# Kernel tuning notes

Measured on AMD Instinct MI355X. Metric: run time of the kernel, lower is better.

The kernel has to match this reference:

```python
import jax, jax.numpy as jnp
import numpy as np

NEG_SLOPE = 0.2  # PyG GATConv default negative_slope


def gat_layer(x, W, a_src, a_dst, bias, src, dst, num_nodes):
    # x: [N, Fin], W: [Fin, H*C], a_src/a_dst: [H, C], bias: [C]
    H, C = a_src.shape
    h = (x @ W).reshape(num_nodes, H, C)                      # [N, H, C]
    alpha_src = jnp.einsum('nhc,hc->nh', h, a_src)            # [N, H]
    alpha_dst = jnp.einsum('nhc,hc->nh', h, a_dst)            # [N, H]
    e = jax.nn.leaky_relu(alpha_src[src] + alpha_dst[dst], NEG_SLOPE)  # [E, H]
    # segment softmax over incoming edges of each destination node
    m = jax.ops.segment_max(e, dst, num_segments=num_nodes)  # [N, H]
    p = jnp.exp(e - m[dst])
    denom = jax.ops.segment_sum(p, dst, num_segments=num_nodes)
    alpha = p / denom[dst]                                    # [E, H]
    out = jax.ops.segment_sum(h[src] * alpha[:, :, None], dst,
                              num_segments=num_nodes)         # [N, H, C]
    return out.mean(axis=1) + bias                            # concat=False -> mean


def setup_inputs() -> dict:
    key = jax.random.key(0)
    ks = jax.random.split(key, 8)
    N, E, F, H = 20000, 640000, 128, 4
    s = 0.1  # weight init scale
    return {
        'x': jax.random.normal(ks[0], (N, F), jnp.float32),
        'W1': jax.random.normal(ks[1], (F, H * F), jnp.float32) * s,
        'a_src1': jax.random.normal(ks[2], (H, F), jnp.float32) * s,
        'a_dst1': jax.random.normal(ks[3], (H, F), jnp.float32) * s,
        'b1': jnp.zeros((F,), jnp.float32),
        'W2': jax.random.normal(ks[4], (F, F), jnp.float32) * s,
        'a_src2': jax.random.normal(ks[5], (1, F), jnp.float32) * s,
        'a_dst2': jax.random.normal(ks[6], (1, F), jnp.float32) * s,
        'b2': jnp.zeros((F,), jnp.float32),
        'edge_index': jax.random.randint(ks[7], (2, E), 0, N, jnp.int32),
    }


def reference(x, W1, a_src1, a_dst1, b1, W2, a_src2, a_dst2, b2, edge_index):
    N = x.shape[0]
    loop = jnp.arange(N, dtype=edge_index.dtype)  # add_self_loops=True (PyG default)
    src = jnp.concatenate([edge_index[0], loop])
    dst = jnp.concatenate([edge_index[1], loop])
    h = jax.nn.elu(gat_layer(x, W1, a_src1, a_dst1, b1, src, dst, N))
    out = jax.nn.elu(gat_layer(h, W2, a_src2, a_dst2, b2, src, dst, N))
    return out
```

## Files before the change

### kernel.cpp

```cpp
#include <hip/hip_runtime.h>
#include <hip/hip_bf16.h>


typedef short v8s __attribute__((ext_vector_type(8)));
typedef float v4f __attribute__((ext_vector_type(4)));
typedef float v2f __attribute__((ext_vector_type(2)));

template <int K> struct IC { static constexpr int value = K; };

constexpr int MAXD = 128;

__device__ __forceinline__ void bf2x(unsigned int u, float& lo, float& hi) {
    union { unsigned int i; float f; } a, b;
    a.i = u << 16;
    b.i = u & 0xffff0000u;
    lo = a.f;
    hi = b.f;
}
__device__ __forceinline__ v2f bf2p(unsigned int u) {
    union { unsigned int i; float f; } a, b;
    a.i = u << 16;
    b.i = u & 0xffff0000u;
    return (v2f){a.f, b.f};
}
__device__ __forceinline__ unsigned short f2bf(float f) {
    union { float f; unsigned int i; } v;
    v.f = f;
    unsigned int lsb = (v.i >> 16) & 1u;
    v.i += 0x7fffu + lsb;
    return (unsigned short)(v.i >> 16);
}
__device__ __forceinline__ unsigned int pack2(float a, float b) {
    return (unsigned int)f2bf(a) | ((unsigned int)f2bf(b) << 16);
}

__global__ void fused_prep_kernel(const float* __restrict__ x,
                                  const float* __restrict__ W1, const float* __restrict__ W2,
                                  const float* __restrict__ as1v, const float* __restrict__ ad1v,
                                  const float* __restrict__ as2v, const float* __restrict__ ad2v,
                                  unsigned short* __restrict__ xb,
                                  unsigned short* __restrict__ Bt1,
                                  unsigned short* __restrict__ Bt2,
                                  float* __restrict__ wsrc1, float* __restrict__ wdst1,
                                  float* __restrict__ wsrc2, float* __restrict__ wdst2,
                                  int* __restrict__ cnt, int* __restrict__ slot,
                                  float* __restrict__ as2, float* __restrict__ ad2, int N) {
    const int Bcast = (N * 32 + 255) / 256;
    int b = blockIdx.x;
    if (b < Bcast) {
        int i = (b * 256 + threadIdx.x) * 4;
        if (i + 3 < N * 128) {
            float4 v = *(const float4*)&x[i];
            ushort4 o;
            o.x = f2bf(v.x);
            o.y = f2bf(v.y);
            o.z = f2bf(v.z);
            o.w = f2bf(v.w);
            *(ushort4*)&xb[i] = o;
        } else {
            for (; i < N * 128; ++i) xb[i] = f2bf(x[i]);
        }
        return;
    }
    b -= Bcast;
    if (b < 256) {
        int i = b * 256 + threadIdx.x;
        int c = i >> 9;
        int r = i & 511;
        int h = r >> 7, k = r & 127;
        Bt1[i] = f2bf(W1[(size_t)k * 512 + (h << 7) + c] * 0.25f);
        return;
    }
    b -= 256;
    if (b < 64) {
        int i = b * 256 + threadIdx.x;
        int c = i >> 7, k = i & 127;
        Bt2[i] = f2bf(W2[(size_t)k * 128 + c]);
        return;
    }
    b -= 64;
    if (b < 2) {
        int i = b * 256 + threadIdx.x;
        int h = i >> 7, k = i & 127;
        const float* wr = W1 + (size_t)k * 512 + (h << 7);
        const float* as_ = as1v + (h << 7);
        const float* ad_ = ad1v + (h << 7);
        float s1 = 0.f, s2 = 0.f;
        for (int c = 0; c < 128; ++c) {
            float wv = wr[c];
            s1 += wv * as_[c];
            s2 += wv * ad_[c];
        }
        wsrc1[i] = s1;
        wdst1[i] = s2;
        return;
    }
    b -= 2;
    if (b < 1) {
        int k = threadIdx.x;
        if (k < 128) {
            const float* wr = W2 + (size_t)k * 128;
            float s1 = 0.f, s2 = 0.f;
            for (int c = 0; c < 128; ++c) {
                float wv = wr[c];
                s1 += wv * as2v[c];
                s2 += wv * ad2v[c];
            }
            wsrc2[k] = s1;
            wdst2[k] = s2;
        }
        return;
    }
    b -= 1;
    {
        int i = b * 256 + threadIdx.x;
        if (i < N) {
            cnt[i] = 1;
            slot[(size_t)i * MAXD] = i;
            as2[i] = 0.f;
            ad2[i] = 0.f;
        }
    }
}

__launch_bounds__(256)
__global__ void fill_alpha_kernel(const int* __restrict__ src, const int* __restrict__ dst,
                                  int* __restrict__ cnt, int* __restrict__ slot, int E,
                                  const unsigned int* __restrict__ xrow,
                                  const float* __restrict__ wsrc, const float* __restrict__ wdst,
                                  float* __restrict__ asrc, float* __restrict__ adst, int N,
                                  int Bfill) {
    if ((int)blockIdx.x < Bfill) {
        int i = (blockIdx.x * 256 + threadIdx.x) * 4;
        if (i + 3 < E) {
            int4 s4 = *(const int4*)&src[i];
            int4 d4 = *(const int4*)&dst[i];
            int p0 = atomicAdd(&cnt[d4.x], 1);
            int p1 = atomicAdd(&cnt[d4.y], 1);
            int p2 = atomicAdd(&cnt[d4.z], 1);
            int p3 = atomicAdd(&cnt[d4.w], 1);
            if (p0 < MAXD) slot[(size_t)d4.x * MAXD + p0] = s4.x;
            if (p1 < MAXD) slot[(size_t)d4.y * MAXD + p1] = s4.y;
            if (p2 < MAXD) slot[(size_t)d4.z * MAXD + p2] = s4.z;
            if (p3 < MAXD) slot[(size_t)d4.w * MAXD + p3] = s4.w;
        } else {
            for (; i < E; ++i) {
                int d = dst[i];
                int pos = atomicAdd(&cnt[d], 1);
                if (pos < MAXD) slot[(size_t)d * MAXD + pos] = src[i];
            }
        }
        return;
    }
    constexpr int H = 4;
    __shared__ float s_wv[2 * H * 128];
    for (int i = threadIdx.x; i < 2 * H * 128; i += 256)
        s_wv[i] = (i < H * 128) ? wsrc[i] : wdst[i - H * 128];
    __syncthreads();
    const int wid = threadIdx.x >> 6, lane = threadIdx.x & 63;
    const int n = (blockIdx.x - Bfill) * 4 + wid;
    if (n >= N) return;
    unsigned int u = xrow[(size_t)n * 64 + lane];
    float f0, f1;
    bf2x(u, f0, f1);
    float s1[H], s2[H];
#pragma unroll
    for (int h = 0; h < H; ++h) {
        float2 ws = *(const float2*)&s_wv[h * 128 + 2 * lane];
        float2 wd = *(const float2*)&s_wv[H * 128 + h * 128 + 2 * lane];
        s1[h] = f0 * ws.x + f1 * ws.y;
        s2[h] = f0 * wd.x + f1 * wd.y;
    }
#pragma unroll
    for (int off = 32; off; off >>= 1)
#pragma unroll
        for (int h = 0; h < H; ++h) {
            s1[h] += __shfl_xor(s1[h], off);
            s2[h] += __shfl_xor(s2[h], off);
        }
    if (lane == 0) {
#pragma unroll
        for (int h = 0; h < H; ++h) {
            asrc[(size_t)n * H + h] = s1[h];
            adst[(size_t)n * H + h] = s2[h];
        }
    }
}

template <int H, int NPB>
__launch_bounds__(64 * NPB, 4)
__global__ void gat_gather_kernel(const uint4* __restrict__ xrow4,
                                  const float* __restrict__ asrc,
                                  const float* __restrict__ adst,
                                  const int* __restrict__ cnt,
                                  const int* __restrict__ slot,
                                  uint4* __restrict__ Sb4,
                                  int N) {
    static_assert(H == 4 || H == 1, "H");
    const int wid = threadIdx.x >> 6, lane = threadIdx.x & 63;
    const int q = lane >> 4, l16 = lane & 15;
    const int n = blockIdx.x * NPB + wid;
    if (n >= N) return;

    __shared__ int s_src_all[NPB][64];
    __shared__ float s_w_all[NPB][64 * H];
    int* s_src = s_src_all[wid];
    float* s_w = s_w_all[wid];

    const int base = n * MAXD;
    const int deg = min(cnt[n], MAXD);

    float adst_n[H];
#pragma unroll
    for (int h = 0; h < H; ++h) adst_n[h] = adst[(size_t)n * H + h];

    float sum_h[H] = {};
    v2f acc[4 * H];
#pragma unroll
    for (int i = 0; i < 4 * H; ++i) acc[i] = (v2f){0.f, 0.f};

    auto do_batch = [&](int j0, auto kc) {
        constexpr int KK = decltype(kc)::value;
        int ss[KK];
        uint4 d[KK];
#pragma unroll
        for (int k = 0; k < KK; ++k) ss[k] = s_src[j0 + k * 4 + q];
#pragma unroll
        for (int k = 0; k < KK; ++k) d[k] = xrow4[(size_t)ss[k] * 16 + l16];
#pragma unroll
        for (int k = 0; k < KK; ++k) {
            v2f f2[4];
            f2[0] = bf2p(d[k].x);
            f2[1] = bf2p(d[k].y);
            f2[2] = bf2p(d[k].z);
            f2[3] = bf2p(d[k].w);
            if constexpr (H == 4) {
                float4 w = *(const float4*)&s_w[(j0 + k * 4 + q) * 4];
                v2f w0 = (v2f){w.x, w.x}, w1 = (v2f){w.y, w.y};
                v2f w2 = (v2f){w.z, w.z}, w3 = (v2f){w.w, w.w};
#pragma unroll
                for (int j = 0; j < 4; ++j) {
                    acc[j] += w0 * f2[j];
                    acc[4 + j] += w1 * f2[j];
                    acc[8 + j] += w2 * f2[j];
                    acc[12 + j] += w3 * f2[j];
                }
            } else {
                float w = s_w[j0 + k * 4 + q];
                v2f w0 = (v2f){w, w};
#pragma unroll
                for (int j = 0; j < 4; ++j) acc[j] += w0 * f2[j];
            }
        }
    };

    for (int i0 = 0; i0 < deg; i0 += 64) {
        const int cntc = min(64, deg - i0);
        {
            const bool valid = lane < cntc;
            int idx = i0 + (valid ? lane : (cntc - 1));
            int s = slot[base + idx];
            s_src[lane] = s;
            if constexpr (H == 4) {
                float4 av = ((const float4*)asrc)[s];
                float ev[4] = {av.x, av.y, av.z, av.w};
#pragma unroll
                for (int hh = 0; hh < 4; ++hh) {
                    float e = ev[hh] + adst_n[hh];
                    e = e > 0.f ? e : 0.2f * e;
                    float wv = valid ? __expf(e) : 0.f;
                    s_w[lane * 4 + hh] = wv;
                    sum_h[hh] += wv;
                }
            } else {
                float e = asrc[s] + adst_n[0];
                e = e > 0.f ? e : 0.2f * e;
                float wv = valid ? __expf(e) : 0.f;
                s_w[lane] = wv;
                sum_h[0] += wv;
            }
        }
        __threadfence_block();

        int j0 = 0;
        for (; j0 + 32 <= cntc; j0 += 32) do_batch(j0, IC<8>{});
        const int rem = cntc - j0;
        if (rem > 0) {
            switch ((rem + 3) >> 2) {
                case 1: do_batch(j0, IC<1>{}); break;
                case 2: do_batch(j0, IC<2>{}); break;
                case 3: do_batch(j0, IC<3>{}); break;
                case 4: do_batch(j0, IC<4>{}); break;
                case 5: do_batch(j0, IC<5>{}); break;
                case 6: do_batch(j0, IC<6>{}); break;
                case 7: do_batch(j0, IC<7>{}); break;
                default: do_batch(j0, IC<8>{}); break;
            }
        }
    }

#pragma unroll
    for (int i = 0; i < 4 * H; ++i) {
        acc[i][0] += __shfl_xor(acc[i][0], 16);
        acc[i][1] += __shfl_xor(acc[i][1], 16);
        acc[i][0] += __shfl_xor(acc[i][0], 32);
        acc[i][1] += __shfl_xor(acc[i][1], 32);
    }
#pragma unroll
    for (int off = 32; off; off >>= 1)
#pragma unroll
        for (int h = 0; h < H; ++h) sum_h[h] += __shfl_xor(sum_h[h], off);

    if constexpr (H == 4) {
#pragma unroll
        for (int h = 0; h < 4; ++h) {
            if (q == h) {
                float rd = 1.0f / sum_h[h];
                uint4 o;
                o.x = pack2(acc[h * 4 + 0][0] * rd, acc[h * 4 + 0][1] * rd);
                o.y = pack2(acc[h * 4 + 1][0] * rd, acc[h * 4 + 1][1] * rd);
                o.z = pack2(acc[h * 4 + 2][0] * rd, acc[h * 4 + 2][1] * rd);
                o.w = pack2(acc[h * 4 + 3][0] * rd, acc[h * 4 + 3][1] * rd);
                Sb4[(size_t)n * 64 + h * 16 + l16] = o;
            }
        }
    } else {
        if (q == 0) {
            float rd = 1.0f / sum_h[0];
            uint4 o;
            o.x = pack2(acc[0][0] * rd, acc[0][1] * rd);
            o.y = pack2(acc[1][0] * rd, acc[1][1] * rd);
            o.z = pack2(acc[2][0] * rd, acc[2][1] * rd);
            o.w = pack2(acc[3][0] * rd, acc[3][1] * rd);
            Sb4[(size_t)n * 16 + l16] = o;
        }
    }
}

__device__ __forceinline__ void store_out(float* p, float v) { *p = v; }
__device__ __forceinline__ void store_out(unsigned short* p, float v) { *p = f2bf(v); }

template <typename OT, bool ELU, bool FUSE_A2>
__launch_bounds__(256)
__global__ void gemm_bias_act_kernel(const unsigned short* __restrict__ A,
                                     const unsigned short* __restrict__ Bt,
                                     const float* __restrict__ bias,
                                     OT* __restrict__ C,
                                     const float* __restrict__ ws2,
                                     const float* __restrict__ wd2,
                                     float* __restrict__ as2, float* __restrict__ ad2,
                                     int M, int Nout, int K) {
    constexpr int BK = 32;
    __shared__ unsigned short As[64][40];
    __shared__ unsigned short Bs[64][40];

    const int tid = threadIdx.x;
    const int w = tid >> 6;
    const int lane = tid & 63;
    const int m16 = lane & 15;
    const int kg = lane >> 4;
    const int m0 = blockIdx.y * 64;
    const int n0 = blockIdx.x * 64;

    v4f acc[4];
#pragma unroll
    for (int i = 0; i < 4; ++i) acc[i] = (v4f){0.f, 0.f, 0.f, 0.f};

    const int srow = tid >> 2;
    const int sseg = tid & 3;
    const int arow_g = min(m0 + srow, M - 1);
    const unsigned short* Ap = &A[(size_t)arow_g * K + sseg * 8];
    const unsigned short* Bp = &Bt[(size_t)(n0 + srow) * K + sseg * 8];

    for (int k0 = 0; k0 < K; k0 += BK) {
        uint4 av = *(const uint4*)(Ap + k0);
        uint4 bv = *(const uint4*)(Bp + k0);
        __syncthreads();
        *(uint4*)&As[srow][sseg * 8] = av;
        *(uint4*)&Bs[srow][sseg * 8] = bv;
        __syncthreads();
        v8s a = *(const v8s*)&As[w * 16 + m16][kg * 8];
#pragma unroll
        for (int i = 0; i < 4; ++i) {
            v8s b = *(const v8s*)&Bs[i * 16 + m16][kg * 8];
            acc[i] = __builtin_amdgcn_mfma_f32_16x16x32_bf16(a, b, acc[i], 0, 0, 0);
        }
    }

    float pr_s[4] = {}, pr_d[4] = {};
#pragma unroll
    for (int i = 0; i < 4; ++i) {
        const int col = n0 + i * 16 + m16;
        const float bv = bias[col];
        float w2s = 0.f, w2d = 0.f;
        if constexpr (FUSE_A2) {
            w2s = ws2[col];
            w2d = wd2[col];
        }
#pragma unroll
        for (int r = 0; r < 4; ++r) {
            int row = m0 + w * 16 + kg * 4 + r;
            if (row < M) {
                float val = acc[i][r] + bv;
                if constexpr (ELU) val = val > 0.f ? val : (__expf(val) - 1.0f);
                store_out(&C[(size_t)row * Nout + col], val);
                if constexpr (FUSE_A2) {
                    pr_s[r] += val * w2s;
                    pr_d[r] += val * w2d;
                }
            }
        }
    }
    if constexpr (FUSE_A2) {
#pragma unroll
        for (int off = 1; off < 16; off <<= 1)
#pragma unroll
            for (int r = 0; r < 4; ++r) {
                pr_s[r] += __shfl_xor(pr_s[r], off);
                pr_d[r] += __shfl_xor(pr_d[r], off);
            }
        if (m16 == 0) {
#pragma unroll
            for (int r = 0; r < 4; ++r) {
                int row = m0 + w * 16 + kg * 4 + r;
                if (row < M) {
                    atomicAdd(&as2[row], pr_s[r]);
                    atomicAdd(&ad2[row], pr_d[r]);
                }
            }
        }
    }
}


extern "C" void kernel_launch(void* const* d_in, const int* in_sizes, int n_in,
                              void* d_out, int out_size, void* d_ws, size_t ws_size,
                              hipStream_t stream) {
    const float* x = (const float*)d_in[0];
    const float* W1 = (const float*)d_in[1];
    const float* a_src1 = (const float*)d_in[2];
    const float* a_dst1 = (const float*)d_in[3];
    const float* b1 = (const float*)d_in[4];
    const float* W2 = (const float*)d_in[5];
    const float* a_src2 = (const float*)d_in[6];
    const float* a_dst2 = (const float*)d_in[7];
    const float* b2 = (const float*)d_in[8];
    const int* edge = (const int*)d_in[9];
    float* out = (float*)d_out;

    constexpr int F = 128, H = 4;
    const int N = in_sizes[0] / F;
    const int E = in_sizes[9] / 2;

    char* ws = (char*)d_ws;
    size_t o = 0;
    auto take = [&](size_t bytes) {
        char* p = ws + o;
        o = (o + bytes + 255) & ~(size_t)255;
        return p;
    };
    int* cnt = (int*)take((size_t)N * 4);
    int* slot = (int*)take((size_t)N * MAXD * 4);
    unsigned short* xb = (unsigned short*)take((size_t)N * F * 2);
    unsigned short* Bt1 = (unsigned short*)take((size_t)F * H * F * 2);
    unsigned short* Bt2 = (unsigned short*)take((size_t)F * F * 2);
    float* wsrc1 = (float*)take((size_t)H * F * 4);
    float* wdst1 = (float*)take((size_t)H * F * 4);
    float* wsrc2 = (float*)take((size_t)F * 4);
    float* wdst2 = (float*)take((size_t)F * 4);
    float* as1 = (float*)take((size_t)N * H * 4);
    float* ad1 = (float*)take((size_t)N * H * 4);
    unsigned short* Sb1 = (unsigned short*)take((size_t)N * H * F * 2);
    unsigned short* h2b = (unsigned short*)take((size_t)N * F * 2);
    float* as2 = (float*)take((size_t)N * 4);
    float* ad2 = (float*)take((size_t)N * 4);
    unsigned short* S2b = (unsigned short*)take((size_t)N * F * 2);
    (void)ws_size;

    const int* esrc = edge;
    const int* edst = edge + E;

    const int Bcast = (N * 32 + 255) / 256;
    const int Bzero = (N + 255) / 256;
    hipLaunchKernelGGL(fused_prep_kernel, dim3(Bcast + 256 + 64 + 2 + 1 + Bzero), dim3(256), 0,
                       stream, x, W1, W2, a_src1, a_dst1, a_src2, a_dst2, xb, Bt1, Bt2, wsrc1,
                       wdst1, wsrc2, wdst2, cnt, slot, as2, ad2, N);

    const int Bfill = (E / 4 + 255) / 256;
    const int Balpha = (N + 3) / 4;
    hipLaunchKernelGGL(fill_alpha_kernel, dim3(Bfill + Balpha), dim3(256), 0, stream, esrc, edst,
                       cnt, slot, E, (const unsigned int*)xb, wsrc1, wdst1, as1, ad1, N, Bfill);

    hipLaunchKernelGGL((gat_gather_kernel<H, 4>), dim3((N + 3) / 4), dim3(256), 0, stream,
                       (const uint4*)xb, as1, ad1, cnt, slot, (uint4*)Sb1, N);
    hipLaunchKernelGGL((gemm_bias_act_kernel<unsigned short, true, true>),
                       dim3(F / 64, (N + 63) / 64), dim3(256), 0, stream, Sb1, Bt1, b1, h2b,
                       wsrc2, wdst2, as2, ad2, N, F, H * F);

    hipLaunchKernelGGL((gat_gather_kernel<1, 4>), dim3((N + 3) / 4), dim3(256), 0, stream,
                       (const uint4*)h2b, as2, ad2, cnt, slot, (uint4*)S2b, N);
    hipLaunchKernelGGL((gemm_bias_act_kernel<float, true, false>), dim3(F / 64, (N + 63) / 64),
                       dim3(256), 0, stream, S2b, Bt2, b2, out, nullptr, nullptr, nullptr,
                       nullptr, N, F, F);
}
```

Baseline: 206.7 us.

## Build adjacency via two-pass binned counting sort with 16-bit slot indices

Replaces the global-atomic scatter that filled per-destination slot lists with a binned partition: a histogram over 64-node bins, a per-block partition into a bin buffer through shared-memory staging, and a per-bin build step that fills slot lists in LDS and writes them out coalesced. Slot indices shrink to 16-bit, halving slot traffic in both gather kernels. This removes random global atomics and scattered 4-byte writes, but adds two kernel launches and an extra pass over the edges. Packing limits source ids to 15 bits and bins to 11 bits, which holds only for N up to 32768.

```diff
diff --git a/kernel.cpp b/kernel.cpp
--- a/kernel.cpp
+++ b/kernel.cpp
@@ -9,6 +9,8 @@
 template <int K> struct IC { static constexpr int value = K; };
 
 constexpr int MAXD = 128;
+constexpr int EPB = 4096;
+constexpr int BINW = 64;
 
 __device__ __forceinline__ void bf2x(unsigned int u, float& lo, float& hi) {
     union { unsigned int i; float f; } a, b;
@@ -32,6 +34,18 @@
 }
 __device__ __forceinline__ unsigned int pack2(float a, float b) {
     return (unsigned int)f2bf(a) | ((unsigned int)f2bf(b) << 16);
+}
+
+__device__ __forceinline__ void scan512_incl(unsigned int* a, int tid) {
+#pragma unroll
+    for (int off = 1; off < 512; off <<= 1) {
+        unsigned int v0 = (tid >= off) ? a[tid - off] : 0u;
+        unsigned int v1 = a[tid + 256 - off];
+        __syncthreads();
+        a[tid] += v0;
+        a[tid + 256] += v1;
+        __syncthreads();
+    }
 }
 
 __global__ void fused_prep_kernel(const float* __restrict__ x,
@@ -43,8 +57,10 @@
                                   unsigned short* __restrict__ Bt2,
                                   float* __restrict__ wsrc1, float* __restrict__ wdst1,
                                   float* __restrict__ wsrc2, float* __restrict__ wdst2,
-                                  int* __restrict__ cnt, int* __restrict__ slot,
-                                  float* __restrict__ as2, float* __restrict__ ad2, int N) {
+                                  unsigned int* __restrict__ ghist,
+                                  unsigned int* __restrict__ bincur,
+                                  float* __restrict__ as2, float* __restrict__ ad2,
+                                  int N, int NB) {
     const int Bcast = (N * 32 + 255) / 256;
     int b = blockIdx.x;
     if (b < Bcast) {
@@ -115,41 +131,45 @@
     {
         int i = b * 256 + threadIdx.x;
         if (i < N) {
-            cnt[i] = 1;
-            slot[(size_t)i * MAXD] = i;
             as2[i] = 0.f;
             ad2[i] = 0.f;
         }
+        if (i < NB) {
+            ghist[i] = 0u;
+            bincur[i] = 0u;
+        }
     }
 }
 
 __launch_bounds__(256)
-__global__ void fill_alpha_kernel(const int* __restrict__ src, const int* __restrict__ dst,
-                                  int* __restrict__ cnt, int* __restrict__ slot, int E,
+__global__ void hist_alpha_kernel(const int* __restrict__ dst, int E,
+                                  unsigned int* __restrict__ ghist, int NB, int Bh,
                                   const unsigned int* __restrict__ xrow,
                                   const float* __restrict__ wsrc, const float* __restrict__ wdst,
-                                  float* __restrict__ asrc, float* __restrict__ adst, int N,
-                                  int Bfill) {
-    if ((int)blockIdx.x < Bfill) {
-        int i = (blockIdx.x * 256 + threadIdx.x) * 4;
-        if (i + 3 < E) {
-            int4 s4 = *(const int4*)&src[i];
-            int4 d4 = *(const int4*)&dst[i];
-            int p0 = atomicAdd(&cnt[d4.x], 1);
-            int p1 = atomicAdd(&cnt[d4.y], 1);
-            int p2 = atomicAdd(&cnt[d4.z], 1);
-            int p3 = atomicAdd(&cnt[d4.w], 1);
-            if (p0 < MAXD) slot[(size_t)d4.x * MAXD + p0] = s4.x;
-            if (p1 < MAXD) slot[(size_t)d4.y * MAXD + p1] = s4.y;
-            if (p2 < MAXD) slot[(size_t)d4.z * MAXD + p2] = s4.z;
-            if (p3 < MAXD) slot[(size_t)d4.w * MAXD + p3] = s4.w;
-        } else {
-            for (; i < E; ++i) {
-                int d = dst[i];
-                int pos = atomicAdd(&cnt[d], 1);
-                if (pos < MAXD) slot[(size_t)d * MAXD + pos] = src[i];
-            }
-        }
+                                  float* __restrict__ asrc, float* __restrict__ adst, int N) {
+    if ((int)blockIdx.x < Bh) {
+        __shared__ unsigned int bh[512];
+        const int tid = threadIdx.x;
+        bh[tid] = 0u;
+        bh[tid + 256] = 0u;
+        __syncthreads();
+        const int e0 = blockIdx.x * EPB;
+        const int ne = min(EPB, E - e0);
+#pragma unroll
+        for (int k = 0; k < 4; ++k) {
+            int rel = (k * 256 + tid) * 4;
+            if (rel < ne) {
+                int4 d4 = *(const int4*)&dst[e0 + rel];
+                atomicAdd(&bh[(unsigned int)d4.x >> 6], 1u);
+                atomicAdd(&bh[(unsigned int)d4.y >> 6], 1u);
+                atomicAdd(&bh[(unsigned int)d4.z >> 6], 1u);
+                atomicAdd(&bh[(unsigned int)d4.w >> 6], 1u);
+            }
+        }
+        __syncthreads();
+        unsigned int c0 = bh[tid], c1 = bh[tid + 256];
+        if (tid < NB && c0) atomicAdd(&ghist[tid], c0);
+        if (tid + 256 < NB && c1) atomicAdd(&ghist[tid + 256], c1);
         return;
     }
     constexpr int H = 4;
@@ -158,7 +178,7 @@
         s_wv[i] = (i < H * 128) ? wsrc[i] : wdst[i - H * 128];
     __syncthreads();
     const int wid = threadIdx.x >> 6, lane = threadIdx.x & 63;
-    const int n = (blockIdx.x - Bfill) * 4 + wid;
+    const int n = (blockIdx.x - Bh) * 4 + wid;
     if (n >= N) return;
     unsigned int u = xrow[(size_t)n * 64 + lane];
     float f0, f1;
@@ -185,6 +205,109 @@
             adst[(size_t)n * H + h] = s2[h];
         }
     }
+}
+
+__launch_bounds__(256)
+__global__ void csr_partition_kernel(const int* __restrict__ src, const int* __restrict__ dst,
+                                     const unsigned int* __restrict__ ghist,
+                                     unsigned int* __restrict__ bincur,
+                                     unsigned int* __restrict__ binBuf, int E, int NB) {
+    __shared__ unsigned int bh[512];
+    __shared__ unsigned int g[512];
+    __shared__ unsigned int sres[512];
+    __shared__ unsigned int stg[EPB];
+    const int tid = threadIdx.x;
+    const int e0 = blockIdx.x * EPB;
+    const int ne = min(EPB, E - e0);
+    bh[tid] = 0u;
+    bh[tid + 256] = 0u;
+    g[tid] = (tid < NB) ? ghist[tid] : 0u;
+    g[tid + 256] = (tid + 256 < NB) ? ghist[tid + 256] : 0u;
+    __syncthreads();
+
+    unsigned int pk[16], ps[16];
+#pragma unroll
+    for (int k = 0; k < 4; ++k) {
+        int rel = (k * 256 + tid) * 4;
+        if (rel < ne) {
+            int4 s4 = *(const int4*)&src[e0 + rel];
+            int4 d4 = *(const int4*)&dst[e0 + rel];
+            int ss[4] = {s4.x, s4.y, s4.z, s4.w};
+            int dd[4] = {d4.x, d4.y, d4.z, d4.w};
+#pragma unroll
+            for (int j = 0; j < 4; ++j) {
+                unsigned int bin = (unsigned int)dd[j] >> 6;
+                pk[k * 4 + j] = (unsigned int)ss[j] |
+                                (((unsigned int)dd[j] & 63u) << 15) | (bin << 21);
+                ps[k * 4 + j] = atomicAdd(&bh[bin], 1u);
+            }
+        } else {
+#pragma unroll
+            for (int j = 0; j < 4; ++j) pk[k * 4 + j] = 0xffffffffu;
+        }
+    }
+    __syncthreads();
+    unsigned int c0 = bh[tid], c1 = bh[tid + 256];
+    unsigned int r0 = 0u, r1 = 0u;
+    if (tid < NB && c0) r0 = atomicAdd(&bincur[tid], c0);
+    if (tid + 256 < NB && c1) r1 = atomicAdd(&bincur[tid + 256], c1);
+    sres[tid] = r0;
+    sres[tid + 256] = r1;
+    __syncthreads();
+    scan512_incl(bh, tid);
+    scan512_incl(g, tid);
+#pragma unroll
+    for (int k = 0; k < 16; ++k) {
+        unsigned int p = pk[k];
+        if (p != 0xffffffffu) {
+            unsigned int bin = p >> 21;
+            unsigned int lo = bin ? bh[bin - 1] : 0u;
+            stg[lo + ps[k]] = p;
+        }
+    }
+    __syncthreads();
+    for (int j = tid; j < ne; j += 256) {
+        unsigned int p = stg[j];
+        unsigned int bin = p >> 21;
+        unsigned int gst = bin ? g[bin - 1] : 0u;
+        unsigned int lo = bin ? bh[bin - 1] : 0u;
+        binBuf[gst + sres[bin] + (unsigned int)j - lo] = p;
+    }
+}
+
+__launch_bounds__(256)
+__global__ void csr_build_kernel(const unsigned int* __restrict__ ghist,
+                                 const unsigned int* __restrict__ binBuf,
+                                 unsigned short* __restrict__ slot,
+                                 int* __restrict__ cnt, int N, int NB) {
+    __shared__ unsigned int g[512];
+    __shared__ unsigned int scnt[BINW];
+    __shared__ unsigned short sslot[BINW][MAXD];
+    const int tid = threadIdx.x;
+    const int b = blockIdx.x;
+    g[tid] = (tid < NB) ? ghist[tid] : 0u;
+    g[tid + 256] = (tid + 256 < NB) ? ghist[tid + 256] : 0u;
+    if (tid < BINW) {
+        scnt[tid] = 1u;
+        sslot[tid][0] = (unsigned short)(b * BINW + tid);
+    }
+    __syncthreads();
+    scan512_incl(g, tid);
+    const unsigned int lo = b ? g[b - 1] : 0u;
+    const unsigned int hiE = g[b];
+    for (unsigned int j = lo + tid; j < hiE; j += 256) {
+        unsigned int p = binBuf[j];
+        int dl = (int)((p >> 15) & 63u);
+        unsigned int pos = atomicAdd(&scnt[dl], 1u);
+        if (pos < (unsigned int)MAXD) sslot[dl][pos] = (unsigned short)(p & 0x7fffu);
+    }
+    __syncthreads();
+    const int rows = min(BINW, N - b * BINW);
+    const int nq = rows * (MAXD / 8);
+    uint4* gdst = (uint4*)(slot + (size_t)b * BINW * MAXD);
+    const uint4* lsrc = (const uint4*)&sslot[0][0];
+    for (int j = tid; j < nq; j += 256) gdst[j] = lsrc[j];
+    if (tid < rows) cnt[b * BINW + tid] = (int)min(scnt[tid], (unsigned int)MAXD);
 }
 
 template <int H, int NPB>
@@ -193,7 +316,7 @@
                                   const float* __restrict__ asrc,
                                   const float* __restrict__ adst,
                                   const int* __restrict__ cnt,
-                                  const int* __restrict__ slot,
+                                  const unsigned short* __restrict__ slot,
                                   uint4* __restrict__ Sb4,
                                   int N) {
     static_assert(H == 4 || H == 1, "H");
@@ -259,7 +382,7 @@
         {
             const bool valid = lane < cntc;
             int idx = i0 + (valid ? lane : (cntc - 1));
-            int s = slot[base + idx];
+            int s = (int)slot[base + idx];
             s_src[lane] = s;
             if constexpr (H == 4) {
                 float4 av = ((const float4*)asrc)[s];
@@ -451,6 +574,7 @@
     constexpr int F = 128, H = 4;
     const int N = in_sizes[0] / F;
     const int E = in_sizes[9] / 2;
+    const int NB = (N + BINW - 1) / BINW;
 
     char* ws = (char*)d_ws;
     size_t o = 0;
@@ -460,7 +584,10 @@
         return p;
     };
     int* cnt = (int*)take((size_t)N * 4);
-    int* slot = (int*)take((size_t)N * MAXD * 4);
+    unsigned short* slot = (unsigned short*)take((size_t)N * MAXD * 2);
+    unsigned int* ghist = (unsigned int*)take((size_t)NB * 4);
+    unsigned int* bincur = (unsigned int*)take((size_t)NB * 4);
+    unsigned int* binBuf = (unsigned int*)take((size_t)E * 4);
     unsigned short* xb = (unsigned short*)take((size_t)N * F * 2);
     unsigned short* Bt1 = (unsigned short*)take((size_t)F * H * F * 2);
     unsigned short* Bt2 = (unsigned short*)take((size_t)F * F * 2);
@@ -484,12 +611,17 @@
     const int Bzero = (N + 255) / 256;
     hipLaunchKernelGGL(fused_prep_kernel, dim3(Bcast + 256 + 64 + 2 + 1 + Bzero), dim3(256), 0,
                        stream, x, W1, W2, a_src1, a_dst1, a_src2, a_dst2, xb, Bt1, Bt2, wsrc1,
-                       wdst1, wsrc2, wdst2, cnt, slot, as2, ad2, N);
-
-    const int Bfill = (E / 4 + 255) / 256;
+                       wdst1, wsrc2, wdst2, ghist, bincur, as2, ad2, N, NB);
+
+    const int Bh = (E + EPB - 1) / EPB;
     const int Balpha = (N + 3) / 4;
-    hipLaunchKernelGGL(fill_alpha_kernel, dim3(Bfill + Balpha), dim3(256), 0, stream, esrc, edst,
-                       cnt, slot, E, (const unsigned int*)xb, wsrc1, wdst1, as1, ad1, N, Bfill);
+    hipLaunchKernelGGL(hist_alpha_kernel, dim3(Bh + Balpha), dim3(256), 0, stream, edst, E,
+                       ghist, NB, Bh, (const unsigned int*)xb, wsrc1, wdst1, as1, ad1, N);
+
+    hipLaunchKernelGGL(csr_partition_kernel, dim3(Bh), dim3(256), 0, stream, esrc, edst, ghist,
+                       bincur, binBuf, E, NB);
+    hipLaunchKernelGGL(csr_build_kernel, dim3(NB), dim3(256), 0, stream, ghist, binBuf, slot,
+                       cnt, N, NB);
 
     hipLaunchKernelGGL((gat_gather_kernel<H, 4>), dim3((N + 3) / 4), dim3(256), 0, stream,
                        (const uint4*)xb, as1, ad1, cnt, slot, (uint4*)Sb1, N);
```

Result: faster. 197.6 us (-4.4%).
